# Optimization experiments

Hardware: AMD Instinct MI355X
Metric: run time of the kernel (lower is better)

The kernel has to match this reference:

```python
import jax, jax.numpy as jnp
import numpy as np

TEMPERATURE = 0.1
NORMALIZED = True


def _l2norm(x, eps=1e-12):
    # matches F.normalize(p=2, dim=1)
    n = jnp.sqrt(jnp.sum(x * x, axis=1, keepdims=True))
    return x / jnp.maximum(n, eps)


def setup_inputs() -> dict:
    key = jax.random.key(0)
    k1, k2, k3, k4 = jax.random.split(key, 4)
    B, D = 4096, 256
    return {
        "hs": jax.random.normal(k1, (B, D), dtype=jnp.float32),
        "ht0": jax.random.normal(k2, (B, D), dtype=jnp.float32),
        "ht1": jax.random.normal(k3, (B, D), dtype=jnp.float32),
        "labels": jax.random.randint(k4, (B,), 0, 100, dtype=jnp.int64)
        if jax.config.jax_enable_x64 else jax.random.randint(k4, (B,), 0, 100, dtype=jnp.int32),
        "num_views": 2,
    }


def _per_teacher_loss(hs_n, ht_n, mask, logits_mask, batch_size, num_views):
    # features: [N, D] with N = 2B
    features = jnp.concatenate([hs_n, ht_n], axis=0)
    sim = jnp.matmul(features, features.T) / TEMPERATURE          # [N, N]
    exp_logits = jnp.exp(sim) * logits_mask                        # [N, N]
    log_prob = sim - jnp.log(jnp.sum(exp_logits, axis=1, keepdims=True))
    per_inst = -jnp.sum(mask * log_prob, axis=1) / jnp.sum(mask, axis=1)  # [N]
    if num_views > 1:
        per_inst = per_inst.reshape(batch_size, num_views).mean(axis=1)
    return per_inst.mean()


def reference(hs, ht0, ht1, labels, num_views):
    batch_size = labels.shape[0]
    hs = hs.reshape(batch_size, -1)
    ht_list = [ht0.reshape(batch_size, -1), ht1.reshape(batch_size, -1)]
    if NORMALIZED:
        hs = _l2norm(hs)
        ht_list = [_l2norm(ht) for ht in ht_list]

    labels2 = jnp.concatenate([labels, labels])                    # [N]
    mask = (labels2[:, None] == labels2[None, :]).astype(jnp.float32)
    N = 2 * batch_size
    logits_mask = 1.0 - jnp.eye(N, dtype=jnp.float32)              # zero diagonal
    mask = mask * logits_mask

    inter_loss = 0.0
    for ht in ht_list:
        inter_loss = inter_loss + _per_teacher_loss(
            hs, ht, mask, logits_mask, batch_size, num_views)
    return inter_loss / len(ht_list)
```

## Files before the change

kernel.cpp:

```cpp
#include <hip/hip_runtime.h>
#include <hip/hip_bf16.h>

#define B_SIZE 4096
#define D_SIZE 256
#define N_SIZE 8192
#define FSCALE 3.798282555f
#define LN2    0.69314718056f

typedef __attribute__((ext_vector_type(8))) short short8;
typedef __attribute__((ext_vector_type(4))) short short4v;
typedef __attribute__((ext_vector_type(4))) float floatx4;


__device__ __forceinline__ void async16(void* lds, const void* g) {
    __builtin_amdgcn_global_load_lds(
        (const __attribute__((address_space(1))) unsigned int*)g,
        (__attribute__((address_space(3))) unsigned int*)lds, 16, 0, 0);
}

__global__ void norm_kernel(const float* __restrict__ hs,
                            const float* __restrict__ ht0,
                            const float* __restrict__ ht1,
                            __hip_bfloat16* __restrict__ dst,
                            float* __restrict__ zero_region,
                            const int* __restrict__ labels,
                            int* __restrict__ cnt, int* __restrict__ offv,
                            int* __restrict__ idxS) {
    int id  = blockIdx.x;
    int tid = threadIdx.x;
    int gid = id * 256 + tid;
    if (gid < 20482) zero_region[gid] = 0.0f;

    const float* src = (id < 4096) ? (hs + id * D_SIZE)
                     : (id < 8192) ? (ht0 + (id - 4096) * D_SIZE)
                                   : (ht1 + (id - 8192) * D_SIZE);
    float x = src[tid];
    float ss = x * x;
#pragma unroll
    for (int off = 32; off > 0; off >>= 1) ss += __shfl_xor(ss, off);
    __shared__ float wsum[4];
    int wave = tid >> 6, lane = tid & 63;
    if (lane == 0) wsum[wave] = ss;
    __syncthreads();
    float tot = wsum[0] + wsum[1] + wsum[2] + wsum[3];
    float inv = 1.0f / fmaxf(sqrtf(tot), 1e-12f);
    dst[id * D_SIZE + tid] = __float2bfloat16(x * inv * FSCALE);

    if (id == 0) {
        __shared__ int h[128], o[128], ctr[128];
        if (tid < 128) { h[tid] = 0; ctr[tid] = 0; }
        __syncthreads();
        for (int i = tid; i < B_SIZE; i += 256) atomicAdd(&h[labels[i] & 127], 1);
        __syncthreads();
        if (tid == 0) {
            int s = 0;
            for (int c = 0; c < 128; ++c) { o[c] = s; s += h[c]; }
        }
        __syncthreads();
        for (int i = tid; i < B_SIZE; i += 256) {
            int lab = labels[i] & 127;
            int pos = o[lab] + atomicAdd(&ctr[lab], 1);
            idxS[pos] = i;
        }
        if (tid < 128) { cnt[tid] = h[tid]; offv[tid] = o[tid]; }
    }
}

__global__ void gvec_kernel(const __hip_bfloat16* __restrict__ featBase,
                            const int* __restrict__ cnt,
                            const int* __restrict__ off,
                            const int* __restrict__ idxS,
                            float* __restrict__ gOut) {
    const int c   = blockIdx.x & 127;
    const int set = blockIdx.x >> 7;
    const int tid = threadIdx.x;
    const __hip_bfloat16* f = featBase + set * B_SIZE * D_SIZE;
    __shared__ int sIdx[256];
    const int n = cnt[c], o = off[c];
    float acc = 0.0f;
    for (int base = 0; base < n; base += 256) {
        int m = n - base; if (m > 256) m = 256;
        __syncthreads();
        if (tid < m) sIdx[tid] = idxS[o + base + tid];
        __syncthreads();
        for (int k = 0; k < m; ++k)
            acc += __bfloat162float(f[sIdx[k] * D_SIZE + tid]);
    }
    gOut[set * 32768 + c * 256 + tid] = acc;
}

__global__ __launch_bounds__(256, 2)
void sim_kernel(const __hip_bfloat16* __restrict__ featS,
                const __hip_bfloat16* __restrict__ featT0,
                const __hip_bfloat16* __restrict__ featT1,
                float* __restrict__ Sarr) {
    __shared__ __align__(16) unsigned char sB[2][32768];

    const int bid = blockIdx.x;
    const int pb  = (bid & 7) * 115 + (bid >> 3);
    const int t   = (pb >= 528) ? 1 : 0;
    const int p   = t ? (pb - 392) : pb;
    const __hip_bfloat16* featT = t ? featT1 : featT0;

    int R = (int)((sqrtf((float)(8 * p + 1)) - 1.0f) * 0.5f);
    while ((R + 1) * (R + 2) / 2 <= p) ++R;
    while (R * (R + 1) / 2 > p) --R;
    const int C = p - R * (R + 1) / 2;

    const int tid  = threadIdx.x;
    const int w    = tid >> 6;
    const int l    = tid & 63;
    const int quad = l >> 4;
    const int lcol = l & 15;
    const int row_base = R * 256 + w * 64;

    float* tgt = (R < 16) ? (Sarr + 2 * N_SIZE) : (Sarr + t * N_SIZE);

    short8 af[4][8];
#pragma unroll
    for (int rt = 0; rt < 4; ++rt) {
        int arow = row_base + rt * 16 + lcol;
        const __hip_bfloat16* ap = (arow < B_SIZE) ? featS + arow * D_SIZE
                                                   : featT + (arow - B_SIZE) * D_SIZE;
#pragma unroll
        for (int ks = 0; ks < 8; ++ks)
            af[rt][ks] = *reinterpret_cast<const short8*>(ap + ks * 32 + quad * 8);
    }

    float Sp[4][4];
#pragma unroll
    for (int rt = 0; rt < 4; ++rt)
#pragma unroll
        for (int r = 0; r < 4; ++r) Sp[rt][r] = 0.0f;

    const int col0 = C * 256;

    auto stage = [&](int b, int cb) {
        int tb = cb + w * 16;
        const __hip_bfloat16* cp = (tb < B_SIZE) ? featS + tb * D_SIZE
                                                 : featT + (tb - B_SIZE) * D_SIZE;
        const char* gp = (const char*)cp + (l & 15) * 512 + (l >> 4) * 16;
        unsigned char* lp = &sB[b][w * 8192];
#pragma unroll
        for (int ks = 0; ks < 8; ++ks)
            async16(lp + ks * 1024, gp + ks * 64);
    };

    stage(0, col0);

    for (int g = 0; g < 4; ++g) {
        const int buf = g & 1;
        __syncthreads();
        if (g + 1 < 4) stage(buf ^ 1, col0 + (g + 1) * 64);

        const int gcol = col0 + g * 64;
        if (gcol > row_base) continue;
        const bool diag = (gcol == row_base);

        float Cp[4] = {0.f, 0.f, 0.f, 0.f};
#pragma unroll
        for (int up = 0; up < 2; ++up) {
            floatx4 acc[2][4];
#pragma unroll
            for (int j = 0; j < 2; ++j)
#pragma unroll
                for (int rt = 0; rt < 4; ++rt) acc[j][rt] = floatx4{0.f, 0.f, 0.f, 0.f};

            __builtin_amdgcn_s_setprio(1);
#pragma unroll
            for (int ks = 0; ks < 8; ++ks) {
                short8 bf[2];
#pragma unroll
                for (int j = 0; j < 2; ++j)
                    bf[j] = *reinterpret_cast<const short8*>(
                        &sB[buf][(up * 2 + j) * 8192 + ks * 1024 + l * 16]);
#pragma unroll
                for (int j = 0; j < 2; ++j)
#pragma unroll
                    for (int rt = 0; rt < 4; ++rt)
                        acc[j][rt] = __builtin_amdgcn_mfma_f32_16x16x32_bf16(
                            af[rt][ks], bf[j], acc[j][rt], 0, 0, 0);
            }
            __builtin_amdgcn_s_setprio(0);
#pragma unroll
            for (int j = 0; j < 2; ++j)
#pragma unroll
                for (int rt = 0; rt < 4; ++rt)
#pragma unroll
                    for (int r = 0; r < 4; ++r) {
                        float e = exp2f(acc[j][rt][r]);
                        Sp[rt][r] += e;
                        Cp[up * 2 + j] += e;
                    }
        }

        if (!diag) {
#pragma unroll
            for (int u = 0; u < 4; ++u) {
                Cp[u] += __shfl_xor(Cp[u], 16);
                Cp[u] += __shfl_xor(Cp[u], 32);
            }
            if (quad == 0) {
#pragma unroll
                for (int u = 0; u < 4; ++u)
                    atomicAdd(&tgt[gcol + u * 16 + lcol], Cp[u]);
            }
        }
    }

#pragma unroll
    for (int rt = 0; rt < 4; ++rt)
#pragma unroll
        for (int r = 0; r < 4; ++r) {
#pragma unroll
            for (int m = 1; m < 16; m <<= 1) Sp[rt][r] += __shfl_xor(Sp[rt][r], m);
        }
    if (lcol == 0) {
#pragma unroll
        for (int rt = 0; rt < 4; ++rt)
#pragma unroll
            for (int r = 0; r < 4; ++r) {
                int row = row_base + rt * 16 + quad * 4 + r;
                atomicAdd(&tgt[row], Sp[rt][r]);
            }
    }
}

__global__ void rowstat_kernel(const __hip_bfloat16* __restrict__ featS,
                               const __hip_bfloat16* __restrict__ featT0,
                               const __hip_bfloat16* __restrict__ featT1,
                               const int* __restrict__ labels,
                               const float* __restrict__ gAll,
                               const int* __restrict__ cnt,
                               const float* __restrict__ Sarr,
                               float* __restrict__ lossAcc,
                               int* __restrict__ ticket,
                               float* __restrict__ out) {
    __shared__ float wpart[4];
    const float* SS = Sarr + 2 * N_SIZE;
    const int tid = threadIdx.x;
    const int wv  = tid >> 6;
    const int l   = tid & 63;
    const int waveid = blockIdx.x * 4 + wv;
    float psum = 0.0f;

    for (int it = 0; it < 8; ++it) {
        int R = waveid * 8 + it;
        int t = R >> 13;
        int i = R & (N_SIZE - 1);
        const __hip_bfloat16* f = (i < B_SIZE) ? featS + i * D_SIZE
                                : (t ? featT1 : featT0) + (i - B_SIZE) * D_SIZE;
        int lab = labels[i & (B_SIZE - 1)] & 127;
        short4v fb = *reinterpret_cast<const short4v*>(f + l * 4);
        float fx[4];
#pragma unroll
        for (int k = 0; k < 4; ++k) {
            unsigned int u = ((unsigned int)(unsigned short)fb[k]) << 16;
            fx[k] = __uint_as_float(u);
        }
        const float* gS = gAll + lab * 256 + l * 4;
        const float* gT = gAll + (1 + t) * 32768 + lab * 256 + l * 4;
        float dot = 0.f, aii = 0.f;
#pragma unroll
        for (int k = 0; k < 4; ++k) {
            dot += fx[k] * (gS[k] + gT[k]);
            aii += fx[k] * fx[k];
        }
#pragma unroll
        for (int m = 1; m < 64; m <<= 1) {
            dot += __shfl_xor(dot, m);
            aii += __shfl_xor(aii, m);
        }
        if (l == 0) {
            float S = Sarr[t * N_SIZE + i];
            if (i < B_SIZE) S += SS[i];
            float M = 2.0f * (float)cnt[lab] - 1.0f;
            float E = exp2f(aii);
            psum += logf(S - E) - LN2 * (dot - aii) / M;
        }
    }
    if (l == 0) wpart[wv] = psum;
    __syncthreads();
    if (tid == 0) {
        atomicAdd(lossAcc, wpart[0] + wpart[1] + wpart[2] + wpart[3]);
        __threadfence();
        if (atomicAdd(ticket, 1) == 511) {
            float tot = atomicAdd(lossAcc, 0.0f);
            out[0] = tot / 16384.0f;
        }
    }
}

extern "C" void kernel_launch(void* const* d_in, const int* in_sizes, int n_in,
                              void* d_out, int out_size, void* d_ws, size_t ws_size,
                              hipStream_t stream) {
    const float* hs     = (const float*)d_in[0];
    const float* ht0    = (const float*)d_in[1];
    const float* ht1    = (const float*)d_in[2];
    const int*   labels = (const int*)d_in[3];

    char* ws = (char*)d_ws;
    float* Sarr    = (float*)(ws);
    float* lossAcc = (float*)(ws + 81920);
    int*   ticket  = (int*)(ws + 81924);
    int*   cnt     = (int*)(ws + 82432);
    int*   offv    = (int*)(ws + 82944);
    int*   idxS    = (int*)(ws + 83456);
    float* gAll    = (float*)(ws + 99840);
    __hip_bfloat16* featS  = (__hip_bfloat16*)(ws + 524288);
    __hip_bfloat16* featT0 = (__hip_bfloat16*)(ws + 524288 + 2097152);
    __hip_bfloat16* featT1 = (__hip_bfloat16*)(ws + 524288 + 2 * 2097152);

    norm_kernel<<<3 * 4096, 256, 0, stream>>>(hs, ht0, ht1, featS, (float*)ws,
                                              labels, cnt, offv, idxS);
    gvec_kernel<<<384, 256, 0, stream>>>(featS, cnt, offv, idxS, gAll);
    sim_kernel<<<920, 256, 0, stream>>>(featS, featT0, featT1, Sarr);
    rowstat_kernel<<<512, 256, 0, stream>>>(featS, featT0, featT1, labels, gAll, cnt,
                                            Sarr, lossAcc, ticket, (float*)d_out);
}
```

Baseline: 153.5 us.

## Use per-wave 16-column triangular tiling with private LDS double buffers in sim kernel

The sim kernel now has each wave stage its own 16-column slices of the column block into a private LDS double buffer. It waits on vmcnt only, with no block-wide barriers. Each wave walks just the column groups up to its own diagonal, so wasted MFMA and exp work on the upper triangle is cut at 16-column rather than 64-column granularity. The trade-off is more loop iterations with less work per iteration and more atomics for column sums. The change also relies on per-wave async LDS ordering being correct without a barrier.

```diff
diff --git a/kernel.cpp b/kernel.cpp
--- a/kernel.cpp
+++ b/kernel.cpp
@@ -94,7 +94,7 @@
                 const __hip_bfloat16* __restrict__ featT0,
                 const __hip_bfloat16* __restrict__ featT1,
                 float* __restrict__ Sarr) {
-    __shared__ __align__(16) unsigned char sB[2][32768];
+    __shared__ __align__(16) unsigned char sB[65536];
 
     const int bid = blockIdx.x;
     const int pb  = (bid & 7) * 115 + (bid >> 3);
@@ -112,16 +112,20 @@
     const int l    = tid & 63;
     const int quad = l >> 4;
     const int lcol = l & 15;
-    const int row_base = R * 256 + w * 64;
+    const int rb   = R * 256 + w * 64;
 
     float* tgt = (R < 16) ? (Sarr + 2 * N_SIZE) : (Sarr + t * N_SIZE);
 
+    const __hip_bfloat16* rowBase = (R < 16) ? featS + (R * 256) * D_SIZE
+                                             : featT + (R * 256 - B_SIZE) * D_SIZE;
+    const int col0 = C * 256;
+    const __hip_bfloat16* colBase = (C < 16) ? featS + col0 * D_SIZE
+                                             : featT + (col0 - B_SIZE) * D_SIZE;
+
     short8 af[4][8];
 #pragma unroll
     for (int rt = 0; rt < 4; ++rt) {
-        int arow = row_base + rt * 16 + lcol;
-        const __hip_bfloat16* ap = (arow < B_SIZE) ? featS + arow * D_SIZE
-                                                   : featT + (arow - B_SIZE) * D_SIZE;
+        const __hip_bfloat16* ap = rowBase + (w * 64 + rt * 16 + lcol) * D_SIZE;
 #pragma unroll
         for (int ks = 0; ks < 8; ++ks)
             af[rt][ks] = *reinterpret_cast<const short8*>(ap + ks * 32 + quad * 8);
@@ -133,79 +137,61 @@
 #pragma unroll
         for (int r = 0; r < 4; ++r) Sp[rt][r] = 0.0f;
 
-    const int col0 = C * 256;
-
-    auto stage = [&](int b, int cb) {
-        int tb = cb + w * 16;
-        const __hip_bfloat16* cp = (tb < B_SIZE) ? featS + tb * D_SIZE
-                                                 : featT + (tb - B_SIZE) * D_SIZE;
-        const char* gp = (const char*)cp + (l & 15) * 512 + (l >> 4) * 16;
-        unsigned char* lp = &sB[b][w * 8192];
+    unsigned char* myLds = &sB[w * 16384];
+
+    auto stage = [&](int b, int cg) {
+        const char* gp = (const char*)(colBase + cg * 16 * D_SIZE)
+                       + lcol * 512 + quad * 16;
+        unsigned char* lp = myLds + b * 8192;
 #pragma unroll
         for (int ks = 0; ks < 8; ++ks)
             async16(lp + ks * 1024, gp + ks * 64);
     };
 
-    stage(0, col0);
-
-    for (int g = 0; g < 4; ++g) {
-        const int buf = g & 1;
-        __syncthreads();
-        if (g + 1 < 4) stage(buf ^ 1, col0 + (g + 1) * 64);
-
-        const int gcol = col0 + g * 64;
-        if (gcol > row_base) continue;
-        const bool diag = (gcol == row_base);
-
-        float Cp[4] = {0.f, 0.f, 0.f, 0.f};
-#pragma unroll
-        for (int up = 0; up < 2; ++up) {
-            floatx4 acc[2][4];
-#pragma unroll
-            for (int j = 0; j < 2; ++j)
-#pragma unroll
-                for (int rt = 0; rt < 4; ++rt) acc[j][rt] = floatx4{0.f, 0.f, 0.f, 0.f};
-
-            __builtin_amdgcn_s_setprio(1);
-#pragma unroll
-            for (int ks = 0; ks < 8; ++ks) {
-                short8 bf[2];
-#pragma unroll
-                for (int j = 0; j < 2; ++j)
-                    bf[j] = *reinterpret_cast<const short8*>(
-                        &sB[buf][(up * 2 + j) * 8192 + ks * 1024 + l * 16]);
-#pragma unroll
-                for (int j = 0; j < 2; ++j)
-#pragma unroll
-                    for (int rt = 0; rt < 4; ++rt)
-                        acc[j][rt] = __builtin_amdgcn_mfma_f32_16x16x32_bf16(
-                            af[rt][ks], bf[j], acc[j][rt], 0, 0, 0);
+    int ng = (rb + 64 - col0) >> 4;
+    if (ng > 16) ng = 16;
+
+    stage(0, 0);
+    int buf = 0;
+    for (int cg = 0; cg < ng; ++cg) {
+        asm volatile("s_waitcnt vmcnt(0)" ::: "memory");
+        if (cg + 1 < ng) stage(buf ^ 1, cg + 1);
+
+        const int c16 = col0 + cg * 16;
+        const bool sym = (c16 + 16 <= rb);
+
+        floatx4 acc[4];
+#pragma unroll
+        for (int rt = 0; rt < 4; ++rt) acc[rt] = floatx4{0.f, 0.f, 0.f, 0.f};
+
+        __builtin_amdgcn_s_setprio(1);
+#pragma unroll
+        for (int ks = 0; ks < 8; ++ks) {
+            short8 bf = *reinterpret_cast<const short8*>(
+                myLds + buf * 8192 + ks * 1024 + l * 16);
+#pragma unroll
+            for (int rt = 0; rt < 4; ++rt)
+                acc[rt] = __builtin_amdgcn_mfma_f32_16x16x32_bf16(
+                    af[rt][ks], bf, acc[rt], 0, 0, 0);
+        }
+        __builtin_amdgcn_s_setprio(0);
+
+        float Cp = 0.0f;
+#pragma unroll
+        for (int rt = 0; rt < 4; ++rt)
+#pragma unroll
+            for (int r = 0; r < 4; ++r) {
+                float e = exp2f(acc[rt][r]);
+                Sp[rt][r] += e;
+                Cp += e;
             }
-            __builtin_amdgcn_s_setprio(0);
-#pragma unroll
-            for (int j = 0; j < 2; ++j)
-#pragma unroll
-                for (int rt = 0; rt < 4; ++rt)
-#pragma unroll
-                    for (int r = 0; r < 4; ++r) {
-                        float e = exp2f(acc[j][rt][r]);
-                        Sp[rt][r] += e;
-                        Cp[up * 2 + j] += e;
-                    }
-        }
-
-        if (!diag) {
-#pragma unroll
-            for (int u = 0; u < 4; ++u) {
-                Cp[u] += __shfl_xor(Cp[u], 16);
-                Cp[u] += __shfl_xor(Cp[u], 32);
-            }
-            if (quad == 0) {
-#pragma unroll
-                for (int u = 0; u < 4; ++u)
-                    atomicAdd(&tgt[gcol + u * 16 + lcol], Cp[u]);
-            }
-        }
+
+        if (sym) {
+            Cp += __shfl_xor(Cp, 16);
+            Cp += __shfl_xor(Cp, 32);
+            if (quad == 0) atomicAdd(&tgt[c16 + lcol], Cp);
+        }
+        buf ^= 1;
     }
 
 #pragma unroll
@@ -220,7 +206,7 @@
         for (int rt = 0; rt < 4; ++rt)
 #pragma unroll
             for (int r = 0; r < 4; ++r) {
-                int row = row_base + rt * 16 + quad * 4 + r;
+                int row = rb + rt * 16 + quad * 4 + r;
                 atomicAdd(&tgt[row], Sp[rt][r]);
             }
     }
```

After: 188.2 us. +22.6%, slower.
